# Optimization experiments

Measured on AMD Instinct MI355X. Metric: run time of the kernel, lower is better.

Reference implementation:

```python
import jax, jax.numpy as jnp
import numpy as np

N, E = 100000, 1600000
D_IN, H1, D1 = 512, 8, 16   # layer0: 8 heads x 16 = hidden 128
H2, D2 = 1, 64              # layer1: 1 head x 64
SLOPE = 0.2


def setup_inputs() -> dict:
    key = jax.random.key(0)
    ks = jax.random.split(key, 9)
    feats = jax.random.normal(ks[0], (N, D_IN), dtype=jnp.float32)
    src = jax.random.randint(ks[1], (E,), 0, N, dtype=jnp.int32)
    dst = jax.random.randint(ks[2], (E,), 0, N, dtype=jnp.int32)
    s = 0.05
    W1 = jax.random.normal(ks[3], (H1 * D1, D_IN), dtype=jnp.float32) * s
    al1 = jax.random.normal(ks[4], (1, H1, D1), dtype=jnp.float32) * s
    ar1 = jax.random.normal(ks[5], (1, H1, D1), dtype=jnp.float32) * s
    W2 = jax.random.normal(ks[6], (H2 * D2, H1 * D1), dtype=jnp.float32) * s
    al2 = jax.random.normal(ks[7], (1, H2, D2), dtype=jnp.float32) * s
    ar2 = jax.random.normal(ks[8], (1, H2, D2), dtype=jnp.float32) * s
    return {"feats": feats, "src": src, "dst": dst,
            "W1": W1, "al1": al1, "ar1": ar1,
            "W2": W2, "al2": al2, "ar2": ar2}


def _segment_softmax(e, seg, n):
    # e: [E, H], softmax over edges sharing the same destination node
    m = jax.ops.segment_max(e, seg, num_segments=n)
    m = jax.lax.stop_gradient(m)
    ex = jnp.exp(e - m[seg])
    s = jax.ops.segment_sum(ex, seg, num_segments=n)
    return ex / s[seg]


def _gat_conv(feat, W, al, ar, src, dst):
    n = feat.shape[0]
    h, d = al.shape[1], al.shape[2]
    ft = (feat @ W.T).reshape(n, h, d)          # [N, H, D]
    el = jnp.sum(ft * al, axis=-1)               # [N, H]
    er = jnp.sum(ft * ar, axis=-1)               # [N, H]
    e = el[src] + er[dst]                        # [E, H]
    e = jnp.where(e >= 0, e, SLOPE * e)          # leaky_relu
    a = _segment_softmax(e, dst, n)              # [E, H]
    msg = ft[src] * a[:, :, None]                # [E, H, D]
    rst = jax.ops.segment_sum(msg, dst, num_segments=n)  # [N, H, D]
    return rst, a


def reference(feats, src, dst, W1, al1, ar1, W2, al2, ar2):
    # layer 0 (activation=relu inside GATConv), then flatten heads
    h1, _ = _gat_conv(feats, W1, al1, ar1, src, dst)
    h1 = jax.nn.relu(h1).reshape(feats.shape[0], -1)    # [N, H1*D1]
    # output layer (1 head, no activation), then mean over heads
    h2, _ = _gat_conv(h1, W2, al2, ar2, src, dst)
    h = h2.mean(axis=1)                                  # [N, D2]
    # forward returns (h_list, h) with h_list = [feats, h1]
    return (feats, h1, h)
```

## Files before the change

### kernel.cpp

```cpp
#include <hip/hip_runtime.h>
#include <math.h>

#define N_NODES 100000
#define N_EDGES 1600000
#define D_IN 512
#define C1 128
#define H1 8
#define D2 64
#define SLOPE 0.2f
#define NB_SCAN 98

typedef unsigned short u16;
typedef unsigned int u32;
typedef u16 u16x4 __attribute__((ext_vector_type(4)));
typedef u16 u16x8 __attribute__((ext_vector_type(8)));
typedef short bf16x8 __attribute__((ext_vector_type(8)));
typedef float f32x4 __attribute__((ext_vector_type(4)));

__device__ __forceinline__ u16 f2bf(float f) {
    unsigned u = __builtin_bit_cast(unsigned, f);
    u += 0x7fffu + ((u >> 16) & 1u);
    return (u16)(u >> 16);
}
__device__ __forceinline__ float bf2f(u16 v) {
    unsigned u = ((unsigned)v) << 16;
    return __builtin_bit_cast(float, u);
}
__device__ __forceinline__ float bflo(u32 u) { return __builtin_bit_cast(float, u << 16); }
__device__ __forceinline__ float bfhi(u32 u) { return __builtin_bit_cast(float, u & 0xffff0000u); }
__device__ __forceinline__ float lrelu(float e) { return e >= 0.f ? e : SLOPE * e; }

__global__ void k_prep_w1(const float* __restrict__ W1, u16* __restrict__ W1b) {
    int i = blockIdx.x * blockDim.x + threadIdx.x;
    float4 v = ((const float4*)W1)[i];
    u16x4 b; b.x = f2bf(v.x); b.y = f2bf(v.y); b.z = f2bf(v.z); b.w = f2bf(v.w);
    ((u16x4*)W1b)[i] = b;
}

__global__ void k_hist(const int* __restrict__ dst, int* __restrict__ cnt) {
    int e = blockIdx.x * blockDim.x + threadIdx.x;
    if (e < N_EDGES) atomicAdd(&cnt[dst[e]], 1);
}

__global__ void k_scan_partials(const int* __restrict__ cnt, int* __restrict__ partials) {
    __shared__ int s[256];
    int t = threadIdx.x;
    int base = blockIdx.x * 1024 + t * 4;
    int sum = 0;
#pragma unroll
    for (int j = 0; j < 4; j++) { int i = base + j; if (i < N_NODES) sum += cnt[i]; }
    s[t] = sum;
    __syncthreads();
    for (int off = 128; off > 0; off >>= 1) {
        if (t < off) s[t] += s[t + off];
        __syncthreads();
    }
    if (t == 0) partials[blockIdx.x] = s[0];
}

__global__ void k_scan_offsets(const int* __restrict__ partials, int* __restrict__ offsets,
                               int* __restrict__ row_start) {
    __shared__ int s[128];
    int t = threadIdx.x;
    int v = (t < NB_SCAN) ? partials[t] : 0;
    s[t] = v;
    __syncthreads();
    for (int off = 1; off < 128; off <<= 1) {
        int x = (t >= off) ? s[t - off] : 0;
        __syncthreads();
        s[t] += x;
        __syncthreads();
    }
    if (t < NB_SCAN) offsets[t] = s[t] - v;
    if (t == NB_SCAN - 1) row_start[N_NODES] = s[t];
}

__global__ void k_scan_final(const int* __restrict__ cnt, const int* __restrict__ offsets,
                             int* __restrict__ row_start, int* __restrict__ cursor) {
    __shared__ int s[256];
    int t = threadIdx.x;
    int base = blockIdx.x * 1024 + t * 4;
    int v[4];
    int sum = 0;
#pragma unroll
    for (int j = 0; j < 4; j++) {
        int i = base + j;
        v[j] = (i < N_NODES) ? cnt[i] : 0;
        sum += v[j];
    }
    s[t] = sum;
    __syncthreads();
    for (int off = 1; off < 256; off <<= 1) {
        int x = (t >= off) ? s[t - off] : 0;
        __syncthreads();
        s[t] += x;
        __syncthreads();
    }
    int b = offsets[blockIdx.x] + s[t] - sum;
    int e = 0;
#pragma unroll
    for (int j = 0; j < 4; j++) {
        int i = base + j;
        if (i < N_NODES) { row_start[i] = b + e; cursor[i] = b + e; }
        e += v[j];
    }
}

__global__ void k_scatter(const int* __restrict__ src, const int* __restrict__ dst,
                          int* __restrict__ cursor, int* __restrict__ csr_src) {
    int e = blockIdx.x * blockDim.x + threadIdx.x;
    if (e < N_EDGES) {
        int pos = atomicAdd(&cursor[dst[e]], 1);
        csr_src[pos] = src[e];
    }
}

__global__ __launch_bounds__(256) void k_gemm1(const float* __restrict__ feats,
                                               const u16* __restrict__ W1b,
                                               const float* __restrict__ al1,
                                               const float* __restrict__ ar1,
                                               u16* __restrict__ ft1b,
                                               float* __restrict__ out0,
                                               float* __restrict__ eler1) {
    __shared__ u16 As[64 * 40];
    __shared__ u16 Bs[128 * 40];
    int t = threadIdx.x;
    int m0 = blockIdx.x * 64;
    int wave = t >> 6, lane = t & 63, quad = lane >> 4, mr = lane & 15;

    f32x4 acc[8];
#pragma unroll
    for (int i = 0; i < 8; i++)
#pragma unroll
        for (int j = 0; j < 4; j++) acc[i][j] = 0.f;

    for (int kt = 0; kt < D_IN; kt += 32) {
        __syncthreads();
#pragma unroll
        for (int l = 0; l < 2; ++l) {
            int idx = t + l * 256;
            int row = idx >> 3, k4 = idx & 7;
            int n = m0 + row;
            float4 v = make_float4(0.f, 0.f, 0.f, 0.f);
            if (n < N_NODES) {
                v = *(const float4*)(feats + (size_t)n * D_IN + kt + k4 * 4);
                *(float4*)(out0 + (size_t)n * D_IN + kt + k4 * 4) = v;
            }
            u16x4 b; b.x = f2bf(v.x); b.y = f2bf(v.y); b.z = f2bf(v.z); b.w = f2bf(v.w);
            *(u16x4*)(As + row * 40 + k4 * 4) = b;
        }
#pragma unroll
        for (int l = 0; l < 2; ++l) {
            int idx = t + l * 256;
            int o = idx >> 2, k8 = idx & 3;
            *(u16x8*)(Bs + o * 40 + k8 * 8) = *(const u16x8*)(W1b + (size_t)o * D_IN + kt + k8 * 8);
        }
        __syncthreads();
        bf16x8 a = *(const bf16x8*)(As + (wave * 16 + mr) * 40 + quad * 8);
#pragma unroll
        for (int nt = 0; nt < 8; ++nt) {
            bf16x8 b = *(const bf16x8*)(Bs + (nt * 16 + mr) * 40 + quad * 8);
            acc[nt] = __builtin_amdgcn_mfma_f32_16x16x32_bf16(a, b, acc[nt], 0, 0, 0);
        }
    }
#pragma unroll
    for (int nt = 0; nt < 8; ++nt)
#pragma unroll
        for (int r = 0; r < 4; ++r) {
            int n = m0 + wave * 16 + quad * 4 + r;
            if (n < N_NODES) ft1b[(size_t)n * C1 + nt * 16 + mr] = f2bf(acc[nt][r]);
        }
    float al1v[8], ar1v[8];
#pragma unroll
    for (int nt = 0; nt < 8; ++nt) { al1v[nt] = al1[nt * 16 + mr]; ar1v[nt] = ar1[nt * 16 + mr]; }
#pragma unroll
    for (int r = 0; r < 4; ++r) {
        int n = m0 + wave * 16 + quad * 4 + r;
        float sel = 0.f;
#pragma unroll
        for (int nt = 0; nt < 8; ++nt) {
            float v = acc[nt][r];
            float pl = v * al1v[nt];
            float pr = v * ar1v[nt];
#pragma unroll
            for (int off = 1; off < 16; off <<= 1) {
                pl += __shfl_xor(pl, off, 64);
                pr += __shfl_xor(pr, off, 64);
            }
            sel = (mr == nt) ? pl : sel;
            sel = (mr == nt + 8) ? pr : sel;
        }
        if (n < N_NODES) eler1[(size_t)n * 16 + mr] = sel;
    }
}

__global__ __launch_bounds__(256) void k_agg1(const u16* __restrict__ ft1b,
                                              const float* __restrict__ eler1,
                                              const int* __restrict__ row_start,
                                              const int* __restrict__ csr_src,
                                              float* __restrict__ h1out,
                                              u32* __restrict__ h1b) {
    int lane = threadIdx.x & 63;
    int n = blockIdx.x * 4 + (threadIdx.x >> 6);
    if (n >= N_NODES) return;
    int h = lane >> 3;
    float era = eler1[(size_t)n * 16 + 8 + h];
    int beg = row_start[n], end = row_start[n + 1];
    float a0 = 0.f, a1 = 0.f, sw = 0.f;
    const u32* ftp = (const u32*)ft1b;
    for (int base = beg; base < end; base += 64) {
        int rem = end - base;
        int sv = csr_src[base + ((lane < rem) ? lane : 0)];
        int cnt = rem < 64 ? rem : 64;
        for (int j = 0; j < cnt; j += 8) {
            int s[8];
#pragma unroll
            for (int kk = 0; kk < 8; ++kk) {
                int idx = j + kk;
                int sl = (idx < cnt) ? idx : j;
                s[kk] = __shfl(sv, sl, 64);
            }
            float e[8];
#pragma unroll
            for (int kk = 0; kk < 8; ++kk) e[kk] = eler1[(size_t)s[kk] * 16 + h];
            u32 f[8];
#pragma unroll
            for (int kk = 0; kk < 8; ++kk) f[kk] = ftp[(size_t)s[kk] * 64 + lane];
#pragma unroll
            for (int kk = 0; kk < 8; ++kk) {
                float w = ((j + kk) < cnt) ? __expf(lrelu(e[kk] + era)) : 0.f;
                a0 = fmaf(w, bflo(f[kk]), a0);
                a1 = fmaf(w, bfhi(f[kk]), a1);
                sw += w;
            }
        }
    }
    float r0 = (sw > 0.f) ? fmaxf(a0 / sw, 0.f) : 0.f;
    float r1 = (sw > 0.f) ? fmaxf(a1 / sw, 0.f) : 0.f;
    float2 rr; rr.x = r0; rr.y = r1;
    *(float2*)(h1out + (size_t)n * C1 + 2 * lane) = rr;
    h1b[n * 64 + lane] = (u32)f2bf(r0) | ((u32)f2bf(r1) << 16);
}

__global__ __launch_bounds__(256) void k_gemm2(const u16* __restrict__ h1b,
                                               const float* __restrict__ W2,
                                               const float* __restrict__ al2,
                                               const float* __restrict__ ar2,
                                               u16* __restrict__ ft2b,
                                               float* __restrict__ el2,
                                               float* __restrict__ er2) {
    __shared__ u16 As[128 * 136];
    __shared__ u16 Bs[64 * 136];
    int t = threadIdx.x;
    int n0 = blockIdx.x * 128;
#pragma unroll
    for (int l = 0; l < 8; ++l) {
        int idx = t + l * 256;
        int row = idx >> 4, c8 = idx & 15;
        int n = n0 + row;
        u16x8 v;
#pragma unroll
        for (int j = 0; j < 8; j++) v[j] = 0;
        if (n < N_NODES) v = *(const u16x8*)(h1b + (size_t)n * C1 + c8 * 8);
        *(u16x8*)(As + row * 136 + c8 * 8) = v;
    }
#pragma unroll
    for (int l = 0; l < 8; ++l) {
        int idx = t + l * 256;
        int o = idx >> 5, k4 = idx & 31;
        float4 w = *(const float4*)(W2 + (size_t)o * C1 + k4 * 4);
        u16x4 b; b.x = f2bf(w.x); b.y = f2bf(w.y); b.z = f2bf(w.z); b.w = f2bf(w.w);
        *(u16x4*)(Bs + o * 136 + k4 * 4) = b;
    }
    __syncthreads();
    int wave = t >> 6, lane = t & 63, quad = lane >> 4, mr = lane & 15;
    f32x4 acc[2][4];
#pragma unroll
    for (int i = 0; i < 2; i++)
#pragma unroll
        for (int j = 0; j < 4; j++)
#pragma unroll
            for (int r = 0; r < 4; r++) acc[i][j][r] = 0.f;
#pragma unroll
    for (int kc = 0; kc < 4; ++kc) {
        bf16x8 a0 = *(const bf16x8*)(As + (wave * 32 + mr) * 136 + kc * 32 + quad * 8);
        bf16x8 a1 = *(const bf16x8*)(As + (wave * 32 + 16 + mr) * 136 + kc * 32 + quad * 8);
#pragma unroll
        for (int nt = 0; nt < 4; ++nt) {
            bf16x8 b = *(const bf16x8*)(Bs + (nt * 16 + mr) * 136 + kc * 32 + quad * 8);
            acc[0][nt] = __builtin_amdgcn_mfma_f32_16x16x32_bf16(a0, b, acc[0][nt], 0, 0, 0);
            acc[1][nt] = __builtin_amdgcn_mfma_f32_16x16x32_bf16(a1, b, acc[1][nt], 0, 0, 0);
        }
    }
#pragma unroll
    for (int mf = 0; mf < 2; ++mf)
#pragma unroll
        for (int nt = 0; nt < 4; ++nt)
#pragma unroll
            for (int r = 0; r < 4; ++r) {
                int n = n0 + wave * 32 + mf * 16 + quad * 4 + r;
                if (n < N_NODES) ft2b[(size_t)n * D2 + nt * 16 + mr] = f2bf(acc[mf][nt][r]);
            }
    float al2v[4], ar2v[4];
#pragma unroll
    for (int nt = 0; nt < 4; ++nt) { al2v[nt] = al2[nt * 16 + mr]; ar2v[nt] = ar2[nt * 16 + mr]; }
#pragma unroll
    for (int mf = 0; mf < 2; ++mf)
#pragma unroll
        for (int r = 0; r < 4; ++r) {
            int n = n0 + wave * 32 + mf * 16 + quad * 4 + r;
            float pl = 0.f, pr = 0.f;
#pragma unroll
            for (int nt = 0; nt < 4; ++nt) {
                float v = acc[mf][nt][r];
                pl = fmaf(v, al2v[nt], pl);
                pr = fmaf(v, ar2v[nt], pr);
            }
#pragma unroll
            for (int off = 1; off < 16; off <<= 1) {
                pl += __shfl_xor(pl, off, 64);
                pr += __shfl_xor(pr, off, 64);
            }
            if (mr == 0 && n < N_NODES) { el2[n] = pl; er2[n] = pr; }
        }
}

__global__ __launch_bounds__(256) void k_agg2(const u16* __restrict__ ft2b,
                                              const float* __restrict__ el2,
                                              const float* __restrict__ er2,
                                              const int* __restrict__ row_start,
                                              const int* __restrict__ csr_src,
                                              float* __restrict__ out2) {
    int lane = threadIdx.x & 63;
    int n = blockIdx.x * 4 + (threadIdx.x >> 6);
    if (n >= N_NODES) return;
    int half = lane >> 5;
    int c = (lane & 31) * 2;
    float ern = er2[n];
    int beg = row_start[n], end = row_start[n + 1];
    float a0 = 0.f, a1 = 0.f, sw = 0.f;
    const u32* ftp = (const u32*)ft2b;
    for (int base = beg; base < end; base += 64) {
        int rem = end - base;
        int sv = csr_src[base + ((lane < rem) ? lane : 0)];
        int cnt = rem < 64 ? rem : 64;
        for (int j = 0; j < cnt; j += 8) {
            int s[4];
#pragma unroll
            for (int kk = 0; kk < 4; ++kk) {
                int idx = j + 2 * kk + half;
                int sl = (idx < cnt) ? idx : j;
                s[kk] = __shfl(sv, sl, 64);
            }
            float e[4];
#pragma unroll
            for (int kk = 0; kk < 4; ++kk) e[kk] = el2[s[kk]];
            u32 f[4];
#pragma unroll
            for (int kk = 0; kk < 4; ++kk) f[kk] = ftp[(size_t)s[kk] * 32 + (lane & 31)];
#pragma unroll
            for (int kk = 0; kk < 4; ++kk) {
                float w = ((j + 2 * kk + half) < cnt) ? __expf(lrelu(e[kk] + ern)) : 0.f;
                a0 = fmaf(w, bflo(f[kk]), a0);
                a1 = fmaf(w, bfhi(f[kk]), a1);
                sw += w;
            }
        }
    }
    a0 += __shfl_xor(a0, 32, 64);
    a1 += __shfl_xor(a1, 32, 64);
    sw += __shfl_xor(sw, 32, 64);
    if (half == 0) {
        float2 rr;
        rr.x = (sw > 0.f) ? a0 / sw : 0.f;
        rr.y = (sw > 0.f) ? a1 / sw : 0.f;
        *(float2*)(out2 + (size_t)n * D2 + c) = rr;
    }
}

extern "C" void kernel_launch(void* const* d_in, const int* in_sizes, int n_in,
                              void* d_out, int out_size, void* d_ws, size_t ws_size,
                              hipStream_t stream) {
    const float* feats = (const float*)d_in[0];
    const int* src = (const int*)d_in[1];
    const int* dst = (const int*)d_in[2];
    const float* W1 = (const float*)d_in[3];
    const float* al1 = (const float*)d_in[4];
    const float* ar1 = (const float*)d_in[5];
    const float* W2 = (const float*)d_in[6];
    const float* al2 = (const float*)d_in[7];
    const float* ar2 = (const float*)d_in[8];

    float* out0 = (float*)d_out;
    float* out1 = out0 + (size_t)N_NODES * D_IN;
    float* out2 = out1 + (size_t)N_NODES * C1;

    char* ws = (char*)d_ws;
    size_t off = 0;
    auto alloc = [&](size_t bytes) -> void* {
        void* p = ws + off;
        off = (off + bytes + 255) & ~(size_t)255;
        return p;
    };
    u16* ft1b = (u16*)alloc((size_t)N_NODES * C1 * 2);
    u16* h1b = (u16*)alloc((size_t)N_NODES * C1 * 2);
    u16* ft2b = (u16*)alloc((size_t)N_NODES * D2 * 2);
    u16* W1b = (u16*)alloc((size_t)C1 * D_IN * 2);
    float* eler1 = (float*)alloc((size_t)N_NODES * 16 * 4);
    float* el2 = (float*)alloc((size_t)N_NODES * 4);
    float* er2 = (float*)alloc((size_t)N_NODES * 4);
    int* cnt = (int*)alloc((size_t)N_NODES * 4);
    int* row_start = (int*)alloc((size_t)(N_NODES + 1) * 4);
    int* cursor = (int*)alloc((size_t)N_NODES * 4);
    int* csr_src = (int*)alloc((size_t)N_EDGES * 4);
    int* partials = (int*)alloc((size_t)NB_SCAN * 4);
    int* offsets = (int*)alloc((size_t)NB_SCAN * 4);

    hipMemsetAsync(cnt, 0, (size_t)N_NODES * 4, stream);
    k_hist<<<(N_EDGES + 255) / 256, 256, 0, stream>>>(dst, cnt);
    k_scan_partials<<<NB_SCAN, 256, 0, stream>>>(cnt, partials);
    k_scan_offsets<<<1, 128, 0, stream>>>(partials, offsets, row_start);
    k_scan_final<<<NB_SCAN, 256, 0, stream>>>(cnt, offsets, row_start, cursor);
    k_scatter<<<(N_EDGES + 255) / 256, 256, 0, stream>>>(src, dst, cursor, csr_src);

    k_prep_w1<<<64, 256, 0, stream>>>(W1, W1b);

    k_gemm1<<<(N_NODES + 63) / 64, 256, 0, stream>>>(feats, W1b, al1, ar1, ft1b, out0, eler1);
    k_agg1<<<(N_NODES + 3) / 4, 256, 0, stream>>>(ft1b, eler1, row_start, csr_src, out1, (u32*)h1b);

    k_gemm2<<<(N_NODES + 127) / 128, 256, 0, stream>>>(h1b, W2, al2, ar2, ft2b, el2, er2);
    k_agg2<<<(N_NODES + 3) / 4, 256, 0, stream>>>(ft2b, el2, er2, row_start, csr_src, out2);
}
```

Measured before the change: 794.3 us.

## Fuse histogram into GEMM1 launch, prefetch tiles, and deepen aggregation unroll

Merges the degree histogram into the first GEMM kernel as extra blocks, so the atomic counting overlaps with the GEMM instead of running as a separate launch. The GEMM now reads W1 in fp32 and converts it to bf16 inside every block, which removes the W1 prep kernel but repeats that conversion per block. Global loads for the next k-tile are issued into registers before the MFMA work on the current tile, a simple software pipeline. Both aggregation kernels unroll the gather loop by 16 instead of 8 to keep more loads in flight, at the cost of more registers.

```diff
diff --git a/kernel.cpp b/kernel.cpp
--- a/kernel.cpp
+++ b/kernel.cpp
@@ -9,6 +9,8 @@
 #define D2 64
 #define SLOPE 0.2f
 #define NB_SCAN 98
+#define G1 1563
+#define NB_HIST 512
 
 typedef unsigned short u16;
 typedef unsigned int u32;
@@ -30,16 +32,109 @@
 __device__ __forceinline__ float bfhi(u32 u) { return __builtin_bit_cast(float, u & 0xffff0000u); }
 __device__ __forceinline__ float lrelu(float e) { return e >= 0.f ? e : SLOPE * e; }
 
-__global__ void k_prep_w1(const float* __restrict__ W1, u16* __restrict__ W1b) {
-    int i = blockIdx.x * blockDim.x + threadIdx.x;
-    float4 v = ((const float4*)W1)[i];
-    u16x4 b; b.x = f2bf(v.x); b.y = f2bf(v.y); b.z = f2bf(v.z); b.w = f2bf(v.w);
-    ((u16x4*)W1b)[i] = b;
-}
-
-__global__ void k_hist(const int* __restrict__ dst, int* __restrict__ cnt) {
-    int e = blockIdx.x * blockDim.x + threadIdx.x;
-    if (e < N_EDGES) atomicAdd(&cnt[dst[e]], 1);
+__global__ __launch_bounds__(256) void k_gemm1_hist(const float* __restrict__ feats,
+                                                    const float* __restrict__ W1,
+                                                    const float* __restrict__ al1,
+                                                    const float* __restrict__ ar1,
+                                                    u16* __restrict__ ft1b,
+                                                    float* __restrict__ out0,
+                                                    float* __restrict__ eler1,
+                                                    const int* __restrict__ dst,
+                                                    int* __restrict__ cnt) {
+    if (blockIdx.x >= G1) {
+        for (int e = (blockIdx.x - G1) * 256 + (int)threadIdx.x; e < N_EDGES;
+             e += NB_HIST * 256)
+            atomicAdd(&cnt[dst[e]], 1);
+        return;
+    }
+    __shared__ u16 As[64 * 40];
+    __shared__ u16 Bs[128 * 40];
+    int t = threadIdx.x;
+    int m0 = blockIdx.x * 64;
+    int wave = t >> 6, lane = t & 63, quad = lane >> 4, mr = lane & 15;
+
+    f32x4 acc[8];
+#pragma unroll
+    for (int i = 0; i < 8; i++)
+#pragma unroll
+        for (int j = 0; j < 4; j++) acc[i][j] = 0.f;
+
+    float4 pa[2], pb[4];
+    auto LOAD = [&](int kt) {
+#pragma unroll
+        for (int l = 0; l < 2; ++l) {
+            int idx = t + l * 256;
+            int row = idx >> 3, k4 = idx & 7;
+            int n = m0 + row;
+            pa[l] = make_float4(0.f, 0.f, 0.f, 0.f);
+            if (n < N_NODES) pa[l] = *(const float4*)(feats + (size_t)n * D_IN + kt + k4 * 4);
+        }
+#pragma unroll
+        for (int l = 0; l < 4; ++l) {
+            int idx = t + l * 256;
+            int o = idx >> 3, k4 = idx & 7;
+            pb[l] = *(const float4*)(W1 + (size_t)o * D_IN + kt + k4 * 4);
+        }
+    };
+    LOAD(0);
+    for (int kt = 0; kt < D_IN; kt += 32) {
+        __syncthreads();
+#pragma unroll
+        for (int l = 0; l < 2; ++l) {
+            int idx = t + l * 256;
+            int row = idx >> 3, k4 = idx & 7;
+            int n = m0 + row;
+            float4 v = pa[l];
+            if (n < N_NODES) *(float4*)(out0 + (size_t)n * D_IN + kt + k4 * 4) = v;
+            u16x4 b; b.x = f2bf(v.x); b.y = f2bf(v.y); b.z = f2bf(v.z); b.w = f2bf(v.w);
+            *(u16x4*)(As + row * 40 + k4 * 4) = b;
+        }
+#pragma unroll
+        for (int l = 0; l < 4; ++l) {
+            int idx = t + l * 256;
+            int o = idx >> 3, k4 = idx & 7;
+            float4 w = pb[l];
+            u16x4 b; b.x = f2bf(w.x); b.y = f2bf(w.y); b.z = f2bf(w.z); b.w = f2bf(w.w);
+            *(u16x4*)(Bs + o * 40 + k4 * 4) = b;
+        }
+        __syncthreads();
+        if (kt + 32 < D_IN) LOAD(kt + 32);
+        bf16x8 a = *(const bf16x8*)(As + (wave * 16 + mr) * 40 + quad * 8);
+#pragma unroll
+        for (int nt = 0; nt < 8; ++nt) {
+            bf16x8 b = *(const bf16x8*)(Bs + (nt * 16 + mr) * 40 + quad * 8);
+            acc[nt] = __builtin_amdgcn_mfma_f32_16x16x32_bf16(a, b, acc[nt], 0, 0, 0);
+        }
+    }
+#pragma unroll
+    for (int nt = 0; nt < 8; ++nt)
+#pragma unroll
+        for (int r = 0; r < 4; ++r) {
+            int n = m0 + wave * 16 + quad * 4 + r;
+            if (n < N_NODES) ft1b[(size_t)n * C1 + nt * 16 + mr] = f2bf(acc[nt][r]);
+        }
+    float al1v[8], ar1v[8];
+#pragma unroll
+    for (int nt = 0; nt < 8; ++nt) { al1v[nt] = al1[nt * 16 + mr]; ar1v[nt] = ar1[nt * 16 + mr]; }
+#pragma unroll
+    for (int r = 0; r < 4; ++r) {
+        int n = m0 + wave * 16 + quad * 4 + r;
+        float sel = 0.f;
+#pragma unroll
+        for (int nt = 0; nt < 8; ++nt) {
+            float v = acc[nt][r];
+            float pl = v * al1v[nt];
+            float pr = v * ar1v[nt];
+#pragma unroll
+            for (int off = 1; off < 16; off <<= 1) {
+                pl += __shfl_xor(pl, off, 64);
+                pr += __shfl_xor(pr, off, 64);
+            }
+            sel = (mr == nt) ? pl : sel;
+            sel = (mr == nt + 8) ? pr : sel;
+        }
+        if (n < N_NODES) eler1[(size_t)n * 16 + mr] = sel;
+    }
 }
 
 __global__ void k_scan_partials(const int* __restrict__ cnt, int* __restrict__ partials) {
@@ -112,85 +207,6 @@
     if (e < N_EDGES) {
         int pos = atomicAdd(&cursor[dst[e]], 1);
         csr_src[pos] = src[e];
-    }
-}
-
-__global__ __launch_bounds__(256) void k_gemm1(const float* __restrict__ feats,
-                                               const u16* __restrict__ W1b,
-                                               const float* __restrict__ al1,
-                                               const float* __restrict__ ar1,
-                                               u16* __restrict__ ft1b,
-                                               float* __restrict__ out0,
-                                               float* __restrict__ eler1) {
-    __shared__ u16 As[64 * 40];
-    __shared__ u16 Bs[128 * 40];
-    int t = threadIdx.x;
-    int m0 = blockIdx.x * 64;
-    int wave = t >> 6, lane = t & 63, quad = lane >> 4, mr = lane & 15;
-
-    f32x4 acc[8];
-#pragma unroll
-    for (int i = 0; i < 8; i++)
-#pragma unroll
-        for (int j = 0; j < 4; j++) acc[i][j] = 0.f;
-
-    for (int kt = 0; kt < D_IN; kt += 32) {
-        __syncthreads();
-#pragma unroll
-        for (int l = 0; l < 2; ++l) {
-            int idx = t + l * 256;
-            int row = idx >> 3, k4 = idx & 7;
-            int n = m0 + row;
-            float4 v = make_float4(0.f, 0.f, 0.f, 0.f);
-            if (n < N_NODES) {
-                v = *(const float4*)(feats + (size_t)n * D_IN + kt + k4 * 4);
-                *(float4*)(out0 + (size_t)n * D_IN + kt + k4 * 4) = v;
-            }
-            u16x4 b; b.x = f2bf(v.x); b.y = f2bf(v.y); b.z = f2bf(v.z); b.w = f2bf(v.w);
-            *(u16x4*)(As + row * 40 + k4 * 4) = b;
-        }
-#pragma unroll
-        for (int l = 0; l < 2; ++l) {
-            int idx = t + l * 256;
-            int o = idx >> 2, k8 = idx & 3;
-            *(u16x8*)(Bs + o * 40 + k8 * 8) = *(const u16x8*)(W1b + (size_t)o * D_IN + kt + k8 * 8);
-        }
-        __syncthreads();
-        bf16x8 a = *(const bf16x8*)(As + (wave * 16 + mr) * 40 + quad * 8);
-#pragma unroll
-        for (int nt = 0; nt < 8; ++nt) {
-            bf16x8 b = *(const bf16x8*)(Bs + (nt * 16 + mr) * 40 + quad * 8);
-            acc[nt] = __builtin_amdgcn_mfma_f32_16x16x32_bf16(a, b, acc[nt], 0, 0, 0);
-        }
-    }
-#pragma unroll
-    for (int nt = 0; nt < 8; ++nt)
-#pragma unroll
-        for (int r = 0; r < 4; ++r) {
-            int n = m0 + wave * 16 + quad * 4 + r;
-            if (n < N_NODES) ft1b[(size_t)n * C1 + nt * 16 + mr] = f2bf(acc[nt][r]);
-        }
-    float al1v[8], ar1v[8];
-#pragma unroll
-    for (int nt = 0; nt < 8; ++nt) { al1v[nt] = al1[nt * 16 + mr]; ar1v[nt] = ar1[nt * 16 + mr]; }
-#pragma unroll
-    for (int r = 0; r < 4; ++r) {
-        int n = m0 + wave * 16 + quad * 4 + r;
-        float sel = 0.f;
-#pragma unroll
-        for (int nt = 0; nt < 8; ++nt) {
-            float v = acc[nt][r];
-            float pl = v * al1v[nt];
-            float pr = v * ar1v[nt];
-#pragma unroll
-            for (int off = 1; off < 16; off <<= 1) {
-                pl += __shfl_xor(pl, off, 64);
-                pr += __shfl_xor(pr, off, 64);
-            }
-            sel = (mr == nt) ? pl : sel;
-            sel = (mr == nt + 8) ? pr : sel;
-        }
-        if (n < N_NODES) eler1[(size_t)n * 16 + mr] = sel;
     }
 }
 
@@ -212,22 +228,22 @@
         int rem = end - base;
         int sv = csr_src[base + ((lane < rem) ? lane : 0)];
         int cnt = rem < 64 ? rem : 64;
-        for (int j = 0; j < cnt; j += 8) {
-            int s[8];
-#pragma unroll
-            for (int kk = 0; kk < 8; ++kk) {
+        for (int j = 0; j < cnt; j += 16) {
+            int s[16];
+#pragma unroll
+            for (int kk = 0; kk < 16; ++kk) {
                 int idx = j + kk;
                 int sl = (idx < cnt) ? idx : j;
                 s[kk] = __shfl(sv, sl, 64);
             }
-            float e[8];
-#pragma unroll
-            for (int kk = 0; kk < 8; ++kk) e[kk] = eler1[(size_t)s[kk] * 16 + h];
-            u32 f[8];
-#pragma unroll
-            for (int kk = 0; kk < 8; ++kk) f[kk] = ftp[(size_t)s[kk] * 64 + lane];
-#pragma unroll
-            for (int kk = 0; kk < 8; ++kk) {
+            float e[16];
+#pragma unroll
+            for (int kk = 0; kk < 16; ++kk) e[kk] = eler1[(size_t)s[kk] * 16 + h];
+            u32 f[16];
+#pragma unroll
+            for (int kk = 0; kk < 16; ++kk) f[kk] = ftp[(size_t)s[kk] * 64 + lane];
+#pragma unroll
+            for (int kk = 0; kk < 16; ++kk) {
                 float w = ((j + kk) < cnt) ? __expf(lrelu(e[kk] + era)) : 0.f;
                 a0 = fmaf(w, bflo(f[kk]), a0);
                 a1 = fmaf(w, bfhi(f[kk]), a1);
@@ -344,22 +360,22 @@
         int rem = end - base;
         int sv = csr_src[base + ((lane < rem) ? lane : 0)];
         int cnt = rem < 64 ? rem : 64;
-        for (int j = 0; j < cnt; j += 8) {
-            int s[4];
-#pragma unroll
-            for (int kk = 0; kk < 4; ++kk) {
+        for (int j = 0; j < cnt; j += 16) {
+            int s[8];
+#pragma unroll
+            for (int kk = 0; kk < 8; ++kk) {
                 int idx = j + 2 * kk + half;
                 int sl = (idx < cnt) ? idx : j;
                 s[kk] = __shfl(sv, sl, 64);
             }
-            float e[4];
-#pragma unroll
-            for (int kk = 0; kk < 4; ++kk) e[kk] = el2[s[kk]];
-            u32 f[4];
-#pragma unroll
-            for (int kk = 0; kk < 4; ++kk) f[kk] = ftp[(size_t)s[kk] * 32 + (lane & 31)];
-#pragma unroll
-            for (int kk = 0; kk < 4; ++kk) {
+            float e[8];
+#pragma unroll
+            for (int kk = 0; kk < 8; ++kk) e[kk] = el2[s[kk]];
+            u32 f[8];
+#pragma unroll
+            for (int kk = 0; kk < 8; ++kk) f[kk] = ftp[(size_t)s[kk] * 32 + (lane & 31)];
+#pragma unroll
+            for (int kk = 0; kk < 8; ++kk) {
                 float w = ((j + 2 * kk + half) < cnt) ? __expf(lrelu(e[kk] + ern)) : 0.f;
                 a0 = fmaf(w, bflo(f[kk]), a0);
                 a1 = fmaf(w, bfhi(f[kk]), a1);
@@ -405,7 +421,6 @@
     u16* ft1b = (u16*)alloc((size_t)N_NODES * C1 * 2);
     u16* h1b = (u16*)alloc((size_t)N_NODES * C1 * 2);
     u16* ft2b = (u16*)alloc((size_t)N_NODES * D2 * 2);
-    u16* W1b = (u16*)alloc((size_t)C1 * D_IN * 2);
     float* eler1 = (float*)alloc((size_t)N_NODES * 16 * 4);
     float* el2 = (float*)alloc((size_t)N_NODES * 4);
     float* er2 = (float*)alloc((size_t)N_NODES * 4);
@@ -417,15 +432,15 @@
     int* offsets = (int*)alloc((size_t)NB_SCAN * 4);
 
     hipMemsetAsync(cnt, 0, (size_t)N_NODES * 4, stream);
-    k_hist<<<(N_EDGES + 255) / 256, 256, 0, stream>>>(dst, cnt);
+
+    k_gemm1_hist<<<G1 + NB_HIST, 256, 0, stream>>>(feats, W1, al1, ar1, ft1b, out0, eler1,
+                                                   dst, cnt);
+
     k_scan_partials<<<NB_SCAN, 256, 0, stream>>>(cnt, partials);
     k_scan_offsets<<<1, 128, 0, stream>>>(partials, offsets, row_start);
     k_scan_final<<<NB_SCAN, 256, 0, stream>>>(cnt, offsets, row_start, cursor);
     k_scatter<<<(N_EDGES + 255) / 256, 256, 0, stream>>>(src, dst, cursor, csr_src);
 
-    k_prep_w1<<<64, 256, 0, stream>>>(W1, W1b);
-
-    k_gemm1<<<(N_NODES + 63) / 64, 256, 0, stream>>>(feats, W1b, al1, ar1, ft1b, out0, eler1);
     k_agg1<<<(N_NODES + 3) / 4, 256, 0, stream>>>(ft1b, eler1, row_start, csr_src, out1, (u32*)h1b);
 
     k_gemm2<<<(N_NODES + 127) / 128, 256, 0, stream>>>(h1b, W2, al2, ar2, ft2b, el2, er2);
```

Measured after the change: 774.9 us. -2.4%, faster.
